# Performance work log

Measured on AMD Instinct MI355X. Metric: run time of the kernel, lower is better.

The kernel has to match this reference:

```python
import jax, jax.numpy as jnp
import numpy as np

B, L, C, H, DK, MAXR = 2, 2048, 256, 8, 32, 7
NEG = jnp.float32(-2**32 + 1)


def _rel_tab(L, maxR):
    # |i-j| with log2 bucketing beyond maxR, clipped to [0, 2*maxR]
    i = jnp.arange(L)
    d = jnp.abs(i[:, None] - i[None, :]).astype(jnp.float32)
    d = jnp.where(d > maxR, maxR + jnp.log2(jnp.maximum(d - maxR, 1.0)), d)
    return jnp.clip(d, 0, 2 * maxR).astype(jnp.int32)  # [L, L]


def setup_inputs() -> dict:
    key = jax.random.key(0)
    ks = jax.random.split(key, 14)
    s = 0.02
    return {
        "qx": jax.random.normal(ks[0], (B, L, C), jnp.float32),
        "kx": jax.random.normal(ks[1], (B, L, C), jnp.float32),
        "vx": jax.random.normal(ks[2], (B, L, C), jnp.float32),
        "preScores": jax.random.normal(ks[3], (B, H, L, L), jnp.float32),
        "maskPAD": jnp.ones((B, L, L), jnp.int32),
        "WQ_w": jax.random.normal(ks[4], (C, H * DK), jnp.float32) * s,
        "WQ_b": jnp.zeros((H * DK,), jnp.float32),
        "WK_w": jax.random.normal(ks[5], (C, H * DK), jnp.float32) * s,
        "WK_b": jnp.zeros((H * DK,), jnp.float32),
        "WV_w": jax.random.normal(ks[6], (C, H * DK), jnp.float32) * s,
        "WV_b": jnp.zeros((H * DK,), jnp.float32),
        "WO_w": jax.random.normal(ks[7], (H * DK, C), jnp.float32) * s,
        "WO_b": jnp.zeros((C,), jnp.float32),
        "embK": jax.random.normal(ks[8], (2 * MAXR + 1, H), jnp.float32),
        "embB": jax.random.normal(ks[9], (2 * MAXR + 1, H), jnp.float32),
    }


def reference(qx, kx, vx, preScores, maskPAD,
              WQ_w, WQ_b, WK_w, WK_b, WV_w, WV_b, WO_w, WO_b, embK, embB):
    q = (qx @ WQ_w + WQ_b).reshape(B, L, H, DK)
    k = (kx @ WK_w + WK_b).reshape(B, L, H, DK)
    v = (vx @ WV_w + WV_b).reshape(B, L, H, DK)
    scores = jnp.einsum('blhd,bmhd->bhlm', q, k) / jnp.float32(np.sqrt(DK))
    tab = _rel_tab(L, MAXR)                       # [L, L] int32
    kb = jnp.transpose(embK[tab], (2, 0, 1))[None]  # [1, H, L, L]
    bb = jnp.transpose(embB[tab], (2, 0, 1))[None]
    scores = scores * kb + bb + preScores
    scores = jnp.where(maskPAD[:, None, :, :] == 0, NEG, scores)
    alpha = jax.nn.softmax(scores, axis=3)        # dropout = identity (eval)
    z = jnp.einsum('bhlm,bmhd->blhd', alpha, v).reshape(B, L, H * DK)
    z = z @ WO_w + WO_b
    return (z, scores)
```

## Files before the change

### kernel.cpp

```cpp
#include <hip/hip_runtime.h>
#include <hip/hip_bf16.h>
#include <math.h>

typedef __bf16 bf16;
typedef __bf16 bf16x8 __attribute__((ext_vector_type(8)));
typedef __bf16 bf16x4 __attribute__((ext_vector_type(4)));
typedef float  f32x4  __attribute__((ext_vector_type(4)));
typedef int    i32x4  __attribute__((ext_vector_type(4)));

#define NB 2
#define NL 2048
#define NC 256
#define NH 8
#define NDK 32
#define JSPLIT 4
#define JCHUNK (NL / JSPLIT)
#define JTILES (JCHUNK / 64)
#define SCALE 0.17677669529663687f
#define NEGV  -4294967296.0f

__global__ __launch_bounds__(256) void proj_kernel(
    const float* __restrict__ qx, const float* __restrict__ kx, const float* __restrict__ vx,
    const float* __restrict__ Wq, const float* __restrict__ bq,
    const float* __restrict__ Wk, const float* __restrict__ bk,
    const float* __restrict__ Wv, const float* __restrict__ bv,
    bf16* __restrict__ qo, bf16* __restrict__ ko, bf16* __restrict__ vto)
{
    const int mode = blockIdx.z;
    const float* X    = (mode == 0) ? qx : (mode == 1) ? kx : vx;
    const float* W    = (mode == 0) ? Wq : (mode == 1) ? Wk : Wv;
    const float* bias = (mode == 0) ? bq : (mode == 1) ? bk : bv;

    __shared__ float As[64][33];
    __shared__ float Bs[32][65];

    const int tid = threadIdx.x;
    const int tx = tid & 15, ty = tid >> 4;
    const int m0 = blockIdx.x * 64, n0 = blockIdx.y * 64;

    float acc[4][4] = {{0.f}};

    for (int k0 = 0; k0 < NC; k0 += 32) {
        const int ar = tid >> 2, ac = (tid & 3) << 3;
        const float4 a0 = *(const float4*)(X + (size_t)(m0 + ar) * NC + k0 + ac);
        const float4 a1 = *(const float4*)(X + (size_t)(m0 + ar) * NC + k0 + ac + 4);
        const int br = tid >> 3, bc = (tid & 7) << 3;
        const float4 b0 = *(const float4*)(W + (size_t)(k0 + br) * NC + n0 + bc);
        const float4 b1 = *(const float4*)(W + (size_t)(k0 + br) * NC + n0 + bc + 4);
        __syncthreads();
        As[ar][ac+0]=a0.x; As[ar][ac+1]=a0.y; As[ar][ac+2]=a0.z; As[ar][ac+3]=a0.w;
        As[ar][ac+4]=a1.x; As[ar][ac+5]=a1.y; As[ar][ac+6]=a1.z; As[ar][ac+7]=a1.w;
        Bs[br][bc+0]=b0.x; Bs[br][bc+1]=b0.y; Bs[br][bc+2]=b0.z; Bs[br][bc+3]=b0.w;
        Bs[br][bc+4]=b1.x; Bs[br][bc+5]=b1.y; Bs[br][bc+6]=b1.z; Bs[br][bc+7]=b1.w;
        __syncthreads();
        #pragma unroll
        for (int kk = 0; kk < 32; ++kk) {
            float av[4], bw[4];
            #pragma unroll
            for (int r = 0; r < 4; ++r) av[r] = As[ty*4+r][kk];
            #pragma unroll
            for (int c = 0; c < 4; ++c) bw[c] = Bs[kk][tx*4+c];
            #pragma unroll
            for (int r = 0; r < 4; ++r)
                #pragma unroll
                for (int c = 0; c < 4; ++c)
                    acc[r][c] = fmaf(av[r], bw[c], acc[r][c]);
        }
    }

    #pragma unroll
    for (int r = 0; r < 4; ++r) {
        const int row = m0 + ty*4 + r;
        const int bb_ = row >> 11, ll = row & (NL - 1);
        #pragma unroll
        for (int c = 0; c < 4; ++c) {
            const int col = n0 + tx*4 + c;
            const float v = acc[r][c] + bias[col];
            const int hh = col >> 5, d = col & 31;
            if (mode == 0)
                qo[(((size_t)bb_*NH + hh)*NL + ll)*NDK + d] = (bf16)v;
            else if (mode == 1)
                ko[(((size_t)bb_*NH + hh)*NL + ll)*NDK + d] = (bf16)v;
            else
                vto[(((size_t)bb_*NH + hh)*NDK + d)*NL + ll] = (bf16)v;
        }
    }
}

__global__ __launch_bounds__(256) void out_gemm_kernel(
    const float* __restrict__ Z, const float* __restrict__ W,
    const float* __restrict__ bias, float* __restrict__ out)
{
    __shared__ float As[32][33];
    __shared__ float Bs[32][65];

    const int tid = threadIdx.x;
    const int tx = tid & 15, ty = tid >> 4;
    const int m0 = blockIdx.x * 32, n0 = blockIdx.y * 64;

    float acc[2][4] = {{0.f}};

    for (int k0 = 0; k0 < NC; k0 += 32) {
        const int ar = tid >> 3, ac = (tid & 7) << 2;
        const float4 a0 = *(const float4*)(Z + (size_t)(m0 + ar) * NC + k0 + ac);
        const int br = tid >> 3, bc = (tid & 7) << 3;
        const float4 b0 = *(const float4*)(W + (size_t)(k0 + br) * NC + n0 + bc);
        const float4 b1 = *(const float4*)(W + (size_t)(k0 + br) * NC + n0 + bc + 4);
        __syncthreads();
        As[ar][ac+0]=a0.x; As[ar][ac+1]=a0.y; As[ar][ac+2]=a0.z; As[ar][ac+3]=a0.w;
        Bs[br][bc+0]=b0.x; Bs[br][bc+1]=b0.y; Bs[br][bc+2]=b0.z; Bs[br][bc+3]=b0.w;
        Bs[br][bc+4]=b1.x; Bs[br][bc+5]=b1.y; Bs[br][bc+6]=b1.z; Bs[br][bc+7]=b1.w;
        __syncthreads();
        #pragma unroll
        for (int kk = 0; kk < 32; ++kk) {
            float av[2], bw[4];
            av[0] = As[ty*2+0][kk];
            av[1] = As[ty*2+1][kk];
            #pragma unroll
            for (int c = 0; c < 4; ++c) bw[c] = Bs[kk][tx*4+c];
            #pragma unroll
            for (int r = 0; r < 2; ++r)
                #pragma unroll
                for (int c = 0; c < 4; ++c)
                    acc[r][c] = fmaf(av[r], bw[c], acc[r][c]);
        }
    }

    #pragma unroll
    for (int r = 0; r < 2; ++r) {
        const int row = m0 + ty*2 + r;
        #pragma unroll
        for (int c = 0; c < 4; ++c) {
            const int col = n0 + tx*4 + c;
            out[(size_t)row * NC + col] = acc[r][c] + bias[col];
        }
    }
}

__global__ __launch_bounds__(256, 4) void attn_kernel(
    const bf16* __restrict__ q, const bf16* __restrict__ k, const bf16* __restrict__ vt,
    const float* __restrict__ preScores, const int* __restrict__ maskPAD,
    const float* __restrict__ embK, const float* __restrict__ embB,
    float* __restrict__ scores_out, float* __restrict__ zp, float2* __restrict__ ml)
{
    const int h  = blockIdx.x & (NH - 1);
    const int i0 = (blockIdx.x >> 3) << 6;
    const int js = blockIdx.y;
    const int b  = blockIdx.z;
    const int tid = threadIdx.x;
    const int lane = tid & 63, w = tid >> 6;
    const int l15 = lane & 15, g = lane >> 4;

    __shared__ __align__(16) bf16 Ks[64][40];
    __shared__ __align__(16) bf16 Vts[32][72];
    __shared__ __align__(16) bf16 Ps[4][16][72];
    __shared__ float2 tab[16];

    if (tid < 15) tab[tid] = make_float2(embK[tid * NH + h], embB[tid * NH + h]);

    const size_t bh = (size_t)b * NH + h;
    const int i_row = i0 + (w << 4) + l15;
    const bf16x8 bQ = *(const bf16x8*)(q + (bh * NL + i_row) * NDK + g * 8);

    const int kr = tid >> 2, kc = (tid & 3) << 3;
    const int vr = tid >> 3, vc = (tid & 7) << 3;
    const bf16* kbase = k  + (bh * NL + kr) * NDK + kc;
    const bf16* vbase = vt + (bh * NDK + vr) * NL + vc;

    const float* preRow   = preScores  + (bh * NL + i_row) * (size_t)NL;
    const int*   maskRow  = maskPAD    + ((size_t)b * NL + i_row) * (size_t)NL;
    float*       scoreRow = scores_out + (bh * NL + i_row) * (size_t)NL;

    f32x4 oF0 = {0.f, 0.f, 0.f, 0.f};
    f32x4 oF1 = {0.f, 0.f, 0.f, 0.f};
    float m_run = -INFINITY, l_run = 0.f;
    const f32x4 zf = {0.f, 0.f, 0.f, 0.f};

    const int jc0 = js * JCHUNK;

    uint4 kv_c = *(const uint4*)(kbase + (size_t)jc0 * NDK);
    uint4 vv_c = *(const uint4*)(vbase + jc0);
    f32x4 pre_c[4]; i32x4 mk_c[4];
    #pragma unroll
    for (int tj = 0; tj < 4; ++tj) {
        const int jb = jc0 + (tj << 4) + (g << 2);
        pre_c[tj] = __builtin_nontemporal_load((const f32x4*)(preRow + jb));
        mk_c[tj]  = *(const i32x4*)(maskRow + jb);
    }

    #pragma unroll
    for (int jt = 0; jt < JTILES; ++jt) {
        const int j0 = jc0 + jt * 64;

        asm volatile("s_waitcnt lgkmcnt(0)" ::: "memory");
        __builtin_amdgcn_s_barrier();
        *(uint4*)&Ks[kr][kc]  = kv_c;
        *(uint4*)&Vts[vr][vc] = vv_c;
        asm volatile("s_waitcnt lgkmcnt(0)" ::: "memory");
        __builtin_amdgcn_s_barrier();

        f32x4 sf[4];
        #pragma unroll
        for (int tj = 0; tj < 4; ++tj) {
            const bf16x8 aK = *(const bf16x8*)&Ks[(tj << 4) | l15][g * 8];
            sf[tj] = __builtin_amdgcn_mfma_f32_16x16x32_bf16(aK, bQ, zf, 0, 0, 0);
        }

        uint4 kv_n, vv_n;
        if (jt + 1 < JTILES) {
            kv_n = *(const uint4*)(kbase + (size_t)(j0 + 64) * NDK);
            vv_n = *(const uint4*)(vbase + (j0 + 64));
        }

        float pmax = -INFINITY;
        #pragma unroll
        for (int tj = 0; tj < 4; ++tj) {
            const int jb = j0 + (tj << 4) + (g << 2);
            f32x4 out4;
            #pragma unroll
            for (int r = 0; r < 4; ++r) {
                const int j = jb + r;
                int dd = i_row - j; dd = dd < 0 ? -dd : dd;
                int idx = dd;
                if (dd > 7) {
                    idx = 38 - __clz(dd - 7);
                    idx = idx > 14 ? 14 : idx;
                }
                const float2 kb2 = tab[idx];
                float sv = sf[tj][r] * SCALE;
                sv = sv * kb2.x + kb2.y + pre_c[tj][r];
                if (mk_c[tj][r] == 0) sv = NEGV;
                out4[r] = sv;
                sf[tj][r] = sv;
                pmax = fmaxf(pmax, sv);
            }
            __builtin_nontemporal_store(out4, (f32x4*)(scoreRow + jb));
        }

        f32x4 pre_n[4]; i32x4 mk_n[4];
        if (jt + 1 < JTILES) {
            #pragma unroll
            for (int tj = 0; tj < 4; ++tj) {
                const int jb = j0 + 64 + (tj << 4) + (g << 2);
                pre_n[tj] = __builtin_nontemporal_load((const f32x4*)(preRow + jb));
                mk_n[tj]  = *(const i32x4*)(maskRow + jb);
            }
        }

        pmax = fmaxf(pmax, __shfl_xor(pmax, 16, 64));
        pmax = fmaxf(pmax, __shfl_xor(pmax, 32, 64));

        const float mn = fmaxf(m_run, pmax);
        const float sc = __expf(m_run - mn);
        m_run = mn;
        float rsum = 0.f;
        #pragma unroll
        for (int tj = 0; tj < 4; ++tj)
            #pragma unroll
            for (int r = 0; r < 4; ++r) {
                const float e = __expf(sf[tj][r] - mn);
                sf[tj][r] = e;
                rsum += e;
            }
        rsum += __shfl_xor(rsum, 16, 64);
        rsum += __shfl_xor(rsum, 32, 64);
        l_run = l_run * sc + rsum;

        #pragma unroll
        for (int r = 0; r < 4; ++r) {
            const float scr = __shfl(sc, 20 * g + r, 64);
            oF0[r] *= scr;
            oF1[r] *= scr;
        }

        #pragma unroll
        for (int tj = 0; tj < 4; ++tj) {
            bf16x4 pk;
            pk[0] = (bf16)sf[tj][0];
            pk[1] = (bf16)sf[tj][1];
            pk[2] = (bf16)sf[tj][2];
            pk[3] = (bf16)sf[tj][3];
            *(bf16x4*)&Ps[w][l15][(tj << 4) | (g << 2)] = pk;
        }
        asm volatile("s_waitcnt lgkmcnt(0)" ::: "memory");

        #pragma unroll
        for (int cc = 0; cc < 2; ++cc) {
            const bf16x8 aP  = *(const bf16x8*)&Ps[w][l15][cc * 32 + g * 8];
            const bf16x8 bV0 = *(const bf16x8*)&Vts[l15][cc * 32 + g * 8];
            const bf16x8 bV1 = *(const bf16x8*)&Vts[16 + l15][cc * 32 + g * 8];
            oF0 = __builtin_amdgcn_mfma_f32_16x16x32_bf16(aP, bV0, oF0, 0, 0, 0);
            oF1 = __builtin_amdgcn_mfma_f32_16x16x32_bf16(aP, bV1, oF1, 0, 0, 0);
        }

        if (jt + 1 < JTILES) {
            kv_c = kv_n; vv_c = vv_n;
            #pragma unroll
            for (int t = 0; t < 4; ++t) { pre_c[t] = pre_n[t]; mk_c[t] = mk_n[t]; }
        }
    }

    #pragma unroll
    for (int r = 0; r < 4; ++r) {
        const int i = i0 + (w << 4) + (g << 2) + r;
        float* zr = zp + ((bh * JSPLIT + js) * (size_t)NL + i) * NDK;
        zr[l15]      = oF0[r];
        zr[16 + l15] = oF1[r];
    }
    if (g == 0)
        ml[(bh * JSPLIT + js) * (size_t)NL + i_row] = make_float2(m_run, l_run);
}

__global__ __launch_bounds__(256) void combine_kernel(
    const float* __restrict__ zp, const float2* __restrict__ ml, float* __restrict__ zbuf)
{
    const int gid = blockIdx.x * 256 + threadIdx.x;
    const int d   = gid & (NDK - 1);
    const int row = gid >> 5;
    const int i   = row & (NL - 1);
    const int bh  = row >> 11;
    const int h   = bh & (NH - 1), b = bh >> 3;

    float m[JSPLIT], l[JSPLIT];
    float M = -INFINITY;
    #pragma unroll
    for (int js = 0; js < JSPLIT; ++js) {
        const float2 t = ml[((size_t)bh * JSPLIT + js) * NL + i];
        m[js] = t.x; l[js] = t.y;
        M = fmaxf(M, t.x);
    }
    float L = 0.f, zs = 0.f;
    #pragma unroll
    for (int js = 0; js < JSPLIT; ++js) {
        const float e = __expf(m[js] - M);
        L += l[js] * e;
        zs = fmaf(zp[(((size_t)bh * JSPLIT + js) * NL + i) * NDK + d], e, zs);
    }
    zbuf[((size_t)b * NL + i) * NC + h * NDK + d] = zs / L;
}

extern "C" void kernel_launch(void* const* d_in, const int* in_sizes, int n_in,
                              void* d_out, int out_size, void* d_ws, size_t ws_size,
                              hipStream_t stream) {
    (void)in_sizes; (void)n_in; (void)out_size; (void)ws_size;

    const float* qx        = (const float*)d_in[0];
    const float* kx        = (const float*)d_in[1];
    const float* vx        = (const float*)d_in[2];
    const float* preScores = (const float*)d_in[3];
    const int*   maskPAD   = (const int*)  d_in[4];
    const float* WQ_w      = (const float*)d_in[5];
    const float* WQ_b      = (const float*)d_in[6];
    const float* WK_w      = (const float*)d_in[7];
    const float* WK_b      = (const float*)d_in[8];
    const float* WV_w      = (const float*)d_in[9];
    const float* WV_b      = (const float*)d_in[10];
    const float* WO_w      = (const float*)d_in[11];
    const float* WO_b      = (const float*)d_in[12];
    const float* embK      = (const float*)d_in[13];
    const float* embB      = (const float*)d_in[14];

    char* ws = (char*)d_ws;
    bf16*   qb   = (bf16*)(ws);
    bf16*   kb   = (bf16*)(ws + (2u << 20));
    bf16*   vtb  = (bf16*)(ws + (4u << 20));
    float*  zbuf = (float*)(ws + (6u << 20));
    float*  zp   = (float*)(ws + (10u << 20));
    float2* mlb  = (float2*)(ws + (26u << 20));

    float* z_out      = (float*)d_out;
    float* scores_out = (float*)d_out + (size_t)NB * NL * NC;

    proj_kernel<<<dim3(64, 4, 3), 256, 0, stream>>>(
        qx, kx, vx, WQ_w, WQ_b, WK_w, WK_b, WV_w, WV_b, qb, kb, vtb);

    attn_kernel<<<dim3((NL / 64) * NH, JSPLIT, NB), 256, 0, stream>>>(
        qb, kb, vtb, preScores, maskPAD, embK, embB, scores_out, zp, mlb);

    combine_kernel<<<dim3((NB * NH * NL * NDK) / 256), 256, 0, stream>>>(zp, mlb, zbuf);

    out_gemm_kernel<<<dim3(NB * NL / 32, 4), 256, 0, stream>>>(zbuf, WO_w, WO_b, z_out);
}
```

Baseline: 236.6 us.

## Load K/V MFMA operands directly from global into registers, drop LDS staging

Removes the shared-memory staging of K and V tiles and the two block-wide barriers per tile. Each lane now loads its own MFMA operand fragments straight from global memory into double-buffered registers, prefetching the next tile. Score stores also change from nontemporal to ordinary stores. This raises register pressure and redundant global/L2 traffic, since each wave fetches the same K/V rows, which may hurt occupancy under the 4-block launch bound.

```diff
diff --git a/kernel.cpp b/kernel.cpp
--- a/kernel.cpp
+++ b/kernel.cpp
@@ -151,21 +151,18 @@
     const int lane = tid & 63, w = tid >> 6;
     const int l15 = lane & 15, g = lane >> 4;
 
-    __shared__ __align__(16) bf16 Ks[64][40];
-    __shared__ __align__(16) bf16 Vts[32][72];
     __shared__ __align__(16) bf16 Ps[4][16][72];
     __shared__ float2 tab[16];
 
     if (tid < 15) tab[tid] = make_float2(embK[tid * NH + h], embB[tid * NH + h]);
+    __syncthreads();
 
     const size_t bh = (size_t)b * NH + h;
     const int i_row = i0 + (w << 4) + l15;
     const bf16x8 bQ = *(const bf16x8*)(q + (bh * NL + i_row) * NDK + g * 8);
 
-    const int kr = tid >> 2, kc = (tid & 3) << 3;
-    const int vr = tid >> 3, vc = (tid & 7) << 3;
-    const bf16* kbase = k  + (bh * NL + kr) * NDK + kc;
-    const bf16* vbase = vt + (bh * NDK + vr) * NL + vc;
+    const bf16* kptr = k  + (bh * NL  + l15) * NDK + (g << 3);
+    const bf16* vptr = vt + (bh * NDK + l15) * NL  + (g << 3);
 
     const float* preRow   = preScores  + (bh * NL + i_row) * (size_t)NL;
     const int*   maskRow  = maskPAD    + ((size_t)b * NL + i_row) * (size_t)NL;
@@ -178,38 +175,41 @@
 
     const int jc0 = js * JCHUNK;
 
-    uint4 kv_c = *(const uint4*)(kbase + (size_t)jc0 * NDK);
-    uint4 vv_c = *(const uint4*)(vbase + jc0);
-    f32x4 pre_c[4]; i32x4 mk_c[4];
+    uint4 kbuf[2][4], vbuf[2][4];
+    f32x4 pbuf[2][4]; i32x4 mbuf[2][4];
+
+    #pragma unroll
+    for (int tj = 0; tj < 4; ++tj)
+        kbuf[0][tj] = *(const uint4*)(kptr + (size_t)(jc0 + tj * 16) * NDK);
+    #pragma unroll
+    for (int cc = 0; cc < 2; ++cc) {
+        vbuf[0][cc*2+0] = *(const uint4*)(vptr + jc0 + cc * 32);
+        vbuf[0][cc*2+1] = *(const uint4*)(vptr + 16 * NL + jc0 + cc * 32);
+    }
     #pragma unroll
     for (int tj = 0; tj < 4; ++tj) {
         const int jb = jc0 + (tj << 4) + (g << 2);
-        pre_c[tj] = __builtin_nontemporal_load((const f32x4*)(preRow + jb));
-        mk_c[tj]  = *(const i32x4*)(maskRow + jb);
+        pbuf[0][tj] = __builtin_nontemporal_load((const f32x4*)(preRow + jb));
+        mbuf[0][tj] = *(const i32x4*)(maskRow + jb);
     }
 
     #pragma unroll
     for (int jt = 0; jt < JTILES; ++jt) {
-        const int j0 = jc0 + jt * 64;
-
-        asm volatile("s_waitcnt lgkmcnt(0)" ::: "memory");
-        __builtin_amdgcn_s_barrier();
-        *(uint4*)&Ks[kr][kc]  = kv_c;
-        *(uint4*)&Vts[vr][vc] = vv_c;
-        asm volatile("s_waitcnt lgkmcnt(0)" ::: "memory");
-        __builtin_amdgcn_s_barrier();
+        const int j0  = jc0 + jt * 64;
+        const int cur = jt & 1;
+        const int nxt = cur ^ 1;
+        const bool more = (jt + 1 < JTILES);
 
         f32x4 sf[4];
         #pragma unroll
-        for (int tj = 0; tj < 4; ++tj) {
-            const bf16x8 aK = *(const bf16x8*)&Ks[(tj << 4) | l15][g * 8];
-            sf[tj] = __builtin_amdgcn_mfma_f32_16x16x32_bf16(aK, bQ, zf, 0, 0, 0);
-        }
-
-        uint4 kv_n, vv_n;
-        if (jt + 1 < JTILES) {
-            kv_n = *(const uint4*)(kbase + (size_t)(j0 + 64) * NDK);
-            vv_n = *(const uint4*)(vbase + (j0 + 64));
+        for (int tj = 0; tj < 4; ++tj)
+            sf[tj] = __builtin_amdgcn_mfma_f32_16x16x32_bf16(
+                __builtin_bit_cast(bf16x8, kbuf[cur][tj]), bQ, zf, 0, 0, 0);
+
+        if (more) {
+            #pragma unroll
+            for (int tj = 0; tj < 4; ++tj)
+                kbuf[nxt][tj] = *(const uint4*)(kptr + (size_t)(j0 + 64 + tj * 16) * NDK);
         }
 
         float pmax = -INFINITY;
@@ -228,22 +228,21 @@
                 }
                 const float2 kb2 = tab[idx];
                 float sv = sf[tj][r] * SCALE;
-                sv = sv * kb2.x + kb2.y + pre_c[tj][r];
-                if (mk_c[tj][r] == 0) sv = NEGV;
+                sv = sv * kb2.x + kb2.y + pbuf[cur][tj][r];
+                if (mbuf[cur][tj][r] == 0) sv = NEGV;
                 out4[r] = sv;
                 sf[tj][r] = sv;
                 pmax = fmaxf(pmax, sv);
             }
-            __builtin_nontemporal_store(out4, (f32x4*)(scoreRow + jb));
-        }
-
-        f32x4 pre_n[4]; i32x4 mk_n[4];
-        if (jt + 1 < JTILES) {
+            *(f32x4*)(scoreRow + jb) = out4;
+        }
+
+        if (more) {
             #pragma unroll
             for (int tj = 0; tj < 4; ++tj) {
                 const int jb = j0 + 64 + (tj << 4) + (g << 2);
-                pre_n[tj] = __builtin_nontemporal_load((const f32x4*)(preRow + jb));
-                mk_n[tj]  = *(const i32x4*)(maskRow + jb);
+                pbuf[nxt][tj] = __builtin_nontemporal_load((const f32x4*)(preRow + jb));
+                mbuf[nxt][tj] = *(const i32x4*)(maskRow + jb);
             }
         }
 
@@ -286,17 +285,19 @@
 
         #pragma unroll
         for (int cc = 0; cc < 2; ++cc) {
-            const bf16x8 aP  = *(const bf16x8*)&Ps[w][l15][cc * 32 + g * 8];
-            const bf16x8 bV0 = *(const bf16x8*)&Vts[l15][cc * 32 + g * 8];
-            const bf16x8 bV1 = *(const bf16x8*)&Vts[16 + l15][cc * 32 + g * 8];
-            oF0 = __builtin_amdgcn_mfma_f32_16x16x32_bf16(aP, bV0, oF0, 0, 0, 0);
-            oF1 = __builtin_amdgcn_mfma_f32_16x16x32_bf16(aP, bV1, oF1, 0, 0, 0);
-        }
-
-        if (jt + 1 < JTILES) {
-            kv_c = kv_n; vv_c = vv_n;
-            #pragma unroll
-            for (int t = 0; t < 4; ++t) { pre_c[t] = pre_n[t]; mk_c[t] = mk_n[t]; }
+            const bf16x8 aP = *(const bf16x8*)&Ps[w][l15][cc * 32 + g * 8];
+            oF0 = __builtin_amdgcn_mfma_f32_16x16x32_bf16(
+                aP, __builtin_bit_cast(bf16x8, vbuf[cur][cc*2+0]), oF0, 0, 0, 0);
+            oF1 = __builtin_amdgcn_mfma_f32_16x16x32_bf16(
+                aP, __builtin_bit_cast(bf16x8, vbuf[cur][cc*2+1]), oF1, 0, 0, 0);
+        }
+
+        if (more) {
+            #pragma unroll
+            for (int cc = 0; cc < 2; ++cc) {
+                vbuf[nxt][cc*2+0] = *(const uint4*)(vptr + j0 + 64 + cc * 32);
+                vbuf[nxt][cc*2+1] = *(const uint4*)(vptr + 16 * NL + j0 + 64 + cc * 32);
+            }
         }
     }
 
```

Result: slower. 257.8 us (+9.0%).
